# Kernel optimization log

Hardware: AMD Instinct MI355X
Metric: run time of the kernel (lower is better)

Reference implementation:

```python
import jax, jax.numpy as jnp
import numpy as np

HIDDEN = 512
HEADS = 8
HEAD_DIM = HIDDEN // HEADS
TB_HID = 32  # temporal-bias MLP hidden width


def setup_inputs() -> dict:
    key = jax.random.key(0)
    ks = jax.random.split(key, 16)
    B, S, D = 4, 1024, HIDDEN
    s = 1.0 / np.sqrt(D)
    inp = {
        "query": jax.random.normal(ks[0], (B, S, D), jnp.float32),
        "key_": jax.random.normal(ks[1], (B, S, D), jnp.float32),
        "value": jax.random.normal(ks[2], (B, S, D), jnp.float32),
        "time_delta": jax.random.uniform(ks[3], (B, S, S), jnp.float32),
        "Wq": jax.random.normal(ks[4], (D, D), jnp.float32) * s,
        "bq": jnp.zeros((D,), jnp.float32),
        "Wk": jax.random.normal(ks[5], (D, D), jnp.float32) * s,
        "bk": jnp.zeros((D,), jnp.float32),
        "Wv": jax.random.normal(ks[6], (D, D), jnp.float32) * s,
        "bv": jnp.zeros((D,), jnp.float32),
        "Wo": jax.random.normal(ks[7], (D, D), jnp.float32) * s,
        "bo": jnp.zeros((D,), jnp.float32),
        "Wt1": jax.random.normal(ks[8], (1, TB_HID), jnp.float32),
        "bt1": jnp.zeros((TB_HID,), jnp.float32),
        "Wt2": jax.random.normal(ks[9], (TB_HID, HEADS), jnp.float32) * (1.0 / np.sqrt(TB_HID)),
        "bt2": jnp.zeros((HEADS,), jnp.float32),
    }
    return inp


def reference(query, key_, value, time_delta,
              Wq, bq, Wk, bk, Wv, bv, Wo, bo, Wt1, bt1, Wt2, bt2):
    B, S, D = query.shape
    H, Hd = HEADS, HEAD_DIM
    scale = jnp.sqrt(jnp.float32(Hd))

    # projections -> [B, H, S, Hd]
    q = (query @ Wq + bq).reshape(B, S, H, Hd).transpose(0, 2, 1, 3)
    k = (key_ @ Wk + bk).reshape(B, S, H, Hd).transpose(0, 2, 1, 3)
    v = (value @ Wv + bv).reshape(B, S, H, Hd).transpose(0, 2, 1, 3)

    # content scores [B, H, S, S]
    scores = jnp.einsum('bhid,bhjd->bhij', q, k) / scale

    # temporal bias: 2-layer MLP on scalar time_delta -> per-head bias
    h = jax.nn.relu(time_delta[..., None] * Wt1[0] + bt1)   # [B, S, S, 32]
    bias = h @ Wt2 + bt2                                    # [B, S, S, H]
    scores = scores + bias.transpose(0, 3, 1, 2)

    attn = jax.nn.softmax(scores, axis=-1)  # dropout = identity (eval)
    out = jnp.einsum('bhij,bhjd->bhid', attn, v)
    out = out.transpose(0, 2, 1, 3).reshape(B, S, D)
    return out @ Wo + bo
```

## Files before the change

### kernel.cpp

```cpp
#include <hip/hip_runtime.h>

typedef _Float16 f16;
typedef _Float16 f16x4 __attribute__((ext_vector_type(4)));
typedef _Float16 f16x8 __attribute__((ext_vector_type(8)));
typedef float f32x4 __attribute__((ext_vector_type(4)));

#define L2E 1.44269504088896340736f

constexpr int D  = 512;
constexpr int S  = 1024;
constexpr int B  = 4;
constexpr int BS = B * S;

constexpr size_t OFF_WT   = 0;
constexpr size_t OFF_Q16  = OFF_WT  + 4ull * D * D * 2;
constexpr size_t OFF_K16  = OFF_Q16 + (size_t)BS * D * 2;
constexpr size_t OFF_VT   = OFF_K16 + (size_t)BS * D * 2;
constexpr size_t OFF_AT   = OFF_VT  + (size_t)BS * D * 2;
constexpr size_t OFF_TAB  = OFF_AT  + (size_t)BS * D * 2;
constexpr size_t OFF_COEF = OFF_TAB + 8ull * 1032 * 4;
constexpr size_t OFF_TDH  = OFF_COEF + 256;

__global__ __launch_bounds__(256) void prep(
    const float* __restrict__ Wq, const float* __restrict__ Wk,
    const float* __restrict__ Wv, const float* __restrict__ Wo,
    f16* __restrict__ WT,
    const float* __restrict__ td, f16* __restrict__ tdh,
    const float* __restrict__ Wt1, const float* __restrict__ bt1,
    const float* __restrict__ Wt2, const float* __restrict__ bt2,
    float* __restrict__ tab, float* __restrict__ coef)
{
    __shared__ float tile[64][65];
    __shared__ float w1s[32], b1s[32], w2s[256], b2s[8];

    const int bx = blockIdx.x;
    const int t = threadIdx.x;

    if (bx < 256) {
        const int z = bx >> 6, xy = bx & 63;
        const float* __restrict__ W = (z == 0) ? Wq : (z == 1) ? Wk : (z == 2) ? Wv : Wo;
        f16* __restrict__ out = WT + (size_t)z * D * D;
        const int k0 = (xy >> 3) * 64, n0 = (xy & 7) * 64;
        for (int i = t; i < 4096; i += 256) {
            int r = i >> 6, c = i & 63;
            tile[r][c] = W[(size_t)(k0 + r) * D + n0 + c];
        }
        __syncthreads();
        for (int i = t; i < 4096; i += 256) {
            int nn = i >> 6, kk = i & 63;
            out[(size_t)(n0 + nn) * D + k0 + kk] = (f16)tile[kk][nn];
        }
    } else if (bx < 2304) {
        const int chunk = (bx - 256) * 256 + t;
        const int row = chunk >> 7;
        const int c7 = chunk & 127;
        const int tl = c7 >> 2, gg = c7 & 3;
        const float* __restrict__ src = td + (size_t)row * S + tl * 32;
        float4 a = *reinterpret_cast<const float4*>(src + gg * 4);
        float4 c = *reinterpret_cast<const float4*>(src + 16 + gg * 4);
        f16x8 hv;
        hv[0] = (f16)a.x; hv[1] = (f16)a.y; hv[2] = (f16)a.z; hv[3] = (f16)a.w;
        hv[4] = (f16)c.x; hv[5] = (f16)c.y; hv[6] = (f16)c.z; hv[7] = (f16)c.w;
        *reinterpret_cast<f16x8*>(tdh + (size_t)chunk * 8) = hv;
    } else {
        if (t < 32) { w1s[t] = Wt1[t]; b1s[t] = bt1[t]; }
        w2s[t] = Wt2[t];
        if (t < 8) b2s[t] = bt2[t];
        __syncthreads();

        const int hh = t >> 5, j = t & 31;

        float f0 = b2s[hh], f1 = b2s[hh];
#pragma unroll 4
        for (int jj = 0; jj < 32; ++jj) {
            float w2 = w2s[jj * 8 + hh];
            f0 += fmaxf(b1s[jj], 0.f) * w2;
            f1 += fmaxf(w1s[jj] + b1s[jj], 0.f) * w2;
        }

        float devj = 0.f;
        {
            float w1 = w1s[j], b1 = b1s[j];
            float u = (w1 != 0.f) ? (-b1 / w1) : -1.f;
            if (u > 0.f && u < 1.f) {
                float fu = b2s[hh];
#pragma unroll 4
                for (int jj = 0; jj < 32; ++jj)
                    fu += fmaxf(fmaf(u, w1s[jj], b1s[jj]), 0.f) * w2s[jj * 8 + hh];
                devj = fabsf(fu - fmaf(u, f1 - f0, f0)) * L2E;
            }
        }
#pragma unroll
        for (int m = 1; m < 32; m <<= 1)
            devj = fmaxf(devj, __shfl_xor(devj, m));

        if (j == 0) {
            coef[hh]     = (f1 - f0) * L2E;
            coef[8 + hh] = f0 * L2E;
            ((int*)coef)[16 + hh] = (devj < 1e-4f) ? 1 : 0;
        }

        for (int idx = t; idx <= 1024; idx += 256) {
            float tdv = (float)idx * (1.0f / 1024.0f);
            float acc[8];
#pragma unroll
            for (int h2 = 0; h2 < 8; ++h2) acc[h2] = b2s[h2];
#pragma unroll 4
            for (int jj = 0; jj < 32; ++jj) {
                float hvv = fmaxf(fmaf(tdv, w1s[jj], b1s[jj]), 0.f);
#pragma unroll
                for (int h2 = 0; h2 < 8; ++h2) acc[h2] += hvv * w2s[jj * 8 + h2];
            }
#pragma unroll
            for (int h2 = 0; h2 < 8; ++h2)
                tab[h2 * 1032 + idx] = acc[h2] * L2E;
        }
    }
}

__global__ __launch_bounds__(256) void proj_gemm(
    const float* __restrict__ Aq, const float* __restrict__ Ak, const float* __restrict__ Av,
    const f16* __restrict__ WT,
    const float* __restrict__ bq, const float* __restrict__ bk, const float* __restrict__ bv,
    f16* __restrict__ q16, f16* __restrict__ k16, f16* __restrict__ vT, float qscale)
{
    __shared__ f16 As[2][128][40];
    __shared__ f16 Bs[2][64][40];

    const int z = blockIdx.z;
    const float* __restrict__ A    = (z == 0) ? Aq : (z == 1) ? Ak : Av;
    const float* __restrict__ bias = (z == 0) ? bq : (z == 1) ? bk : bv;
    const f16* __restrict__ W      = WT + (size_t)z * D * D;
    const float scale = (z == 0) ? qscale : 1.0f;

    const int t = threadIdx.x;
    const int l = t & 63, w = t >> 6;
    const int i16 = l & 15, g = l >> 4;
    const int wm = w >> 1, wn = w & 1;
    const int m0 = blockIdx.x * 128, n0 = blockIdx.y * 64;

    f32x4 acc[4][2] = {};

    float4 ar[4];
    f16x8  br;
    const int arow = t >> 3, ac4 = t & 7;
    const int brow = t >> 2, bc8 = t & 3;

    auto load_stage = [&](int kt) {
        const int k0 = kt * 32;
#pragma unroll
        for (int r = 0; r < 4; ++r)
            ar[r] = *reinterpret_cast<const float4*>(A + (size_t)(m0 + arow + 32 * r) * D + k0 + ac4 * 4);
        br = *reinterpret_cast<const f16x8*>(W + (size_t)(n0 + brow) * D + k0 + bc8 * 8);
    };
    auto write_stage = [&](int buf) {
#pragma unroll
        for (int r = 0; r < 4; ++r) {
            f16x4 hv;
            hv[0] = (f16)ar[r].x; hv[1] = (f16)ar[r].y; hv[2] = (f16)ar[r].z; hv[3] = (f16)ar[r].w;
            *reinterpret_cast<f16x4*>(&As[buf][arow + 32 * r][ac4 * 4]) = hv;
        }
        *reinterpret_cast<f16x8*>(&Bs[buf][brow][bc8 * 8]) = br;
    };

    load_stage(0);
    write_stage(0);
    __syncthreads();

    for (int kt = 0; kt < 16; ++kt) {
        const int cur = kt & 1;
        if (kt < 15) load_stage(kt + 1);

        f16x8 af[4], bf[2];
#pragma unroll
        for (int i = 0; i < 4; ++i)
            af[i] = *reinterpret_cast<const f16x8*>(&As[cur][wm * 64 + i * 16 + i16][g * 8]);
#pragma unroll
        for (int j = 0; j < 2; ++j)
            bf[j] = *reinterpret_cast<const f16x8*>(&Bs[cur][wn * 32 + j * 16 + i16][g * 8]);
#pragma unroll
        for (int i = 0; i < 4; ++i)
#pragma unroll
            for (int j = 0; j < 2; ++j)
                acc[i][j] = __builtin_amdgcn_mfma_f32_16x16x32_f16(af[i], bf[j], acc[i][j], 0, 0, 0);

        if (kt < 15) write_stage(cur ^ 1);
        __syncthreads();
    }

    float bvv[2];
#pragma unroll
    for (int j = 0; j < 2; ++j) bvv[j] = bias[n0 + wn * 32 + j * 16 + i16];

    if (z < 2) {
        f16* __restrict__ out = (z == 0) ? q16 : k16;
#pragma unroll
        for (int i = 0; i < 4; ++i) {
#pragma unroll
            for (int j = 0; j < 2; ++j) {
                const int nn = n0 + wn * 32 + j * 16 + i16;
#pragma unroll
                for (int e = 0; e < 4; ++e) {
                    const int mr = m0 + wm * 64 + i * 16 + g * 4 + e;
                    out[(size_t)mr * D + nn] = (f16)((acc[i][j][e] + bvv[j]) * scale);
                }
            }
        }
    } else {
#pragma unroll
        for (int i = 0; i < 4; ++i) {
            const int mr = m0 + wm * 64 + i * 16 + g * 4;
            const int bb = mr >> 10, jj = mr & 1023;
#pragma unroll
            for (int j = 0; j < 2; ++j) {
                const int nn = n0 + wn * 32 + j * 16 + i16;
                f16x4 hv;
#pragma unroll
                for (int e = 0; e < 4; ++e) hv[e] = (f16)(acc[i][j][e] + bvv[j]);
                *reinterpret_cast<f16x4*>(vT + ((size_t)(bb * D + nn)) * S + jj) = hv;
            }
        }
    }
}

__global__ __launch_bounds__(512, 4) void attn_kernel(
    const f16* __restrict__ q16, const f16* __restrict__ k16, const f16* __restrict__ vT,
    const f16* __restrict__ tdh, const float* __restrict__ tabg, const float* __restrict__ coef,
    f16* __restrict__ out16)
{
    __shared__ __align__(16) f16 Ks[2][2][2048];
    __shared__ __align__(16) f16 Vs[2][2][2048];
    __shared__ __align__(16) f16 Ps[8][512];
    __shared__ float obuf[4][16][68];
    __shared__ float mlb[4][2][16];

    const int bid = blockIdx.x;
    const int b  = bid & 3;
    const int h  = (bid >> 2) & 7;
    const int qt = bid >> 5;

    const int t = threadIdx.x;
    const int w = t >> 6, l = t & 63;
    const int i16 = l & 15, g = l >> 4;
    const int half = w >> 2, pr = w & 3;
    const int qrow = qt * 64 + pr * 16 + i16;

    const float cH = coef[h], dH = coef[8 + h];
    const int lin = ((const int*)coef)[16 + h];
    const float* __restrict__ th = tabg + h * 1032;

    f16x8 qf[2];
#pragma unroll
    for (int kf = 0; kf < 2; ++kf)
        qf[kf] = *reinterpret_cast<const f16x8*>(
            q16 + (size_t)(b * S + qrow) * D + h * 64 + kf * 32 + g * 8);

    float mr = -1e30f, lr = 0.f;
    f32x4 o[4] = {};

    const int kh   = t >> 8;
    const int krow = (t >> 3) & 31, kc8 = t & 7;
    const int vdv  = (t >> 2) & 63, vj8 = t & 3;
    const int kofs = krow * 64 + ((kc8 ^ (krow & 7)) << 3);
    const int vofs = vdv * 32 + ((vj8 ^ (vdv & 3)) << 3);
    f16x8 sk, sv;

    auto stage_load = [&](int jt) {
        sk = *reinterpret_cast<const f16x8*>(
            k16 + (size_t)(b * S + kh * 512 + jt * 32 + krow) * D + h * 64 + kc8 * 8);
        sv = *reinterpret_cast<const f16x8*>(
            vT + (size_t)(b * D + h * 64 + vdv) * S + kh * 512 + jt * 32 + vj8 * 8);
    };
    auto stage_write = [&](int buf) {
        *reinterpret_cast<f16x8*>(&Ks[buf][kh][kofs]) = sk;
        *reinterpret_cast<f16x8*>(&Vs[buf][kh][vofs]) = sv;
    };

    int kro0[2], kro1[2], vro[4];
#pragma unroll
    for (int fj = 0; fj < 2; ++fj) {
        const int rj = fj * 16 + i16;
        kro0[fj] = rj * 64 + ((g ^ (i16 & 7)) << 3);
        kro1[fj] = rj * 64 + (((g + 4) ^ (i16 & 7)) << 3);
    }
#pragma unroll
    for (int fv = 0; fv < 4; ++fv)
        vro[fv] = (fv * 16 + i16) * 32 + ((g ^ (i16 & 3)) << 3);

    const int q2  = (i16 >> 1) & 3;
    const int pw0 = i16 * 32 + ((((g >> 1)    ) ^ q2) << 3) + ((g & 1) << 2);
    const int pw1 = i16 * 32 + ((((g >> 1) + 2) ^ q2) << 3) + ((g & 1) << 2);
    const int prd = i16 * 32 + ((g ^ q2) << 3);

    const f16* __restrict__ tdp = tdh + (size_t)(b * S + qrow) * S + half * 512 + g * 8;
    f16x8 tcur, tnext;

    stage_load(0);
    tcur = *reinterpret_cast<const f16x8*>(tdp);
    stage_write(0);
    __syncthreads();

    for (int jt = 0; jt < 16; ++jt) {
        const int cur = jt & 1;
        if (jt < 15) {
            stage_load(jt + 1);
            tnext = *reinterpret_cast<const f16x8*>(tdp + (jt + 1) * 32);
        }

        f32x4 s[2];
#pragma unroll
        for (int fj = 0; fj < 2; ++fj) {
            f16x8 ka0 = *reinterpret_cast<const f16x8*>(&Ks[cur][half][kro0[fj]]);
            f16x8 ka1 = *reinterpret_cast<const f16x8*>(&Ks[cur][half][kro1[fj]]);
            f32x4 zz = {0.f, 0.f, 0.f, 0.f};
            zz = __builtin_amdgcn_mfma_f32_16x16x32_f16(ka0, qf[0], zz, 0, 0, 0);
            s[fj] = __builtin_amdgcn_mfma_f32_16x16x32_f16(ka1, qf[1], zz, 0, 0, 0);
        }

        float pvv[2][4];
        float tmax = -1e30f;
#pragma unroll
        for (int fj = 0; fj < 2; ++fj)
#pragma unroll
            for (int e = 0; e < 4; ++e) {
                float u = (float)tcur[fj * 4 + e];
                float vsc;
                if (lin) {
                    vsc = fmaf(u, cH, s[fj][e] + dH);
                } else {
                    float x = fminf(fmaxf(u, 0.f), 1.f) * 1024.f;
                    int ix = (int)x;
                    ix = (ix > 1023) ? 1023 : ix;
                    float fr = x - (float)ix;
                    float t0v = th[ix], t1v = th[ix + 1];
                    vsc = s[fj][e] + fmaf(fr, t1v - t0v, t0v);
                }
                pvv[fj][e] = vsc;
                tmax = fmaxf(tmax, vsc);
            }
        tmax = fmaxf(tmax, __shfl_xor(tmax, 16));
        tmax = fmaxf(tmax, __shfl_xor(tmax, 32));
        if (__any(tmax > mr)) {
            float mnew = fmaxf(mr, tmax);
            float alpha = exp2f(mr - mnew);
            mr = mnew;
            lr *= alpha;
#pragma unroll
            for (int fv = 0; fv < 4; ++fv) o[fv] *= alpha;
        }

        float rsum = 0.f;
        f16x4 pq[2];
#pragma unroll
        for (int fj = 0; fj < 2; ++fj)
#pragma unroll
            for (int e = 0; e < 4; ++e) {
                float p = exp2f(pvv[fj][e] - mr);
                rsum += p;
                pq[fj][e] = (f16)p;
            }
        rsum += __shfl_xor(rsum, 16);
        rsum += __shfl_xor(rsum, 32);
        lr += rsum;

        f16* ps = Ps[w];
        *reinterpret_cast<f16x4*>(ps + pw0) = pq[0];
        *reinterpret_cast<f16x4*>(ps + pw1) = pq[1];
        f16x8 pb = *reinterpret_cast<const f16x8*>(ps + prd);

#pragma unroll
        for (int fv = 0; fv < 4; ++fv) {
            f16x8 va = *reinterpret_cast<const f16x8*>(&Vs[cur][half][vro[fv]]);
            o[fv] = __builtin_amdgcn_mfma_f32_16x16x32_f16(va, pb, o[fv], 0, 0, 0);
        }

        if (jt < 15) stage_write(cur ^ 1);
        __syncthreads();
        tcur = tnext;
    }

    if (half == 1) {
#pragma unroll
        for (int fv = 0; fv < 4; ++fv)
            *reinterpret_cast<f32x4*>(&obuf[pr][i16][fv * 16 + g * 4]) = o[fv];
        if (g == 0) { mlb[pr][0][i16] = mr; mlb[pr][1][i16] = lr; }
    }
    __syncthreads();
    if (half == 0) {
        const float m1 = mlb[pr][0][i16], l1 = mlb[pr][1][i16];
        const float mm = fmaxf(mr, m1);
        const float a0 = exp2f(mr - mm), a1 = exp2f(m1 - mm);
        const float inv = 1.0f / (lr * a0 + l1 * a1);
#pragma unroll
        for (int fv = 0; fv < 4; ++fv) {
            f32x4 o1 = *reinterpret_cast<const f32x4*>(&obuf[pr][i16][fv * 16 + g * 4]);
            f16x4 hv;
#pragma unroll
            for (int e = 0; e < 4; ++e) hv[e] = (f16)((o[fv][e] * a0 + o1[e] * a1) * inv);
            *reinterpret_cast<f16x4*>(
                out16 + (size_t)(b * S + qrow) * D + h * 64 + fv * 16 + g * 4) = hv;
        }
    }
}

__global__ __launch_bounds__(256) void final_gemm(const f16* __restrict__ A, const f16* __restrict__ WoT,
                                                  const float* __restrict__ bo, float* __restrict__ out)
{
    __shared__ f16 As[2][64][40];
    __shared__ f16 Bs[2][64][40];

    const int t = threadIdx.x;
    const int l = t & 63, w = t >> 6;
    const int i16 = l & 15, g = l >> 4;
    const int wm = w >> 1, wn = w & 1;
    const int m0 = blockIdx.x * 64, n0 = blockIdx.y * 64;

    f32x4 acc[2][2] = {};
    f16x8 ar, br;
    const int srow = t >> 2, sc8 = t & 3;

    auto load_stage = [&](int kt) {
        const int k0 = kt * 32;
        ar = *reinterpret_cast<const f16x8*>(A + (size_t)(m0 + srow) * D + k0 + sc8 * 8);
        br = *reinterpret_cast<const f16x8*>(WoT + (size_t)(n0 + srow) * D + k0 + sc8 * 8);
    };
    auto write_stage = [&](int buf) {
        *reinterpret_cast<f16x8*>(&As[buf][srow][sc8 * 8]) = ar;
        *reinterpret_cast<f16x8*>(&Bs[buf][srow][sc8 * 8]) = br;
    };

    load_stage(0);
    write_stage(0);
    __syncthreads();

    for (int kt = 0; kt < 16; ++kt) {
        const int cur = kt & 1;
        if (kt < 15) load_stage(kt + 1);

        f16x8 af[2], bf[2];
#pragma unroll
        for (int i = 0; i < 2; ++i)
            af[i] = *reinterpret_cast<const f16x8*>(&As[cur][wm * 32 + i * 16 + i16][g * 8]);
#pragma unroll
        for (int j = 0; j < 2; ++j)
            bf[j] = *reinterpret_cast<const f16x8*>(&Bs[cur][wn * 32 + j * 16 + i16][g * 8]);
#pragma unroll
        for (int i = 0; i < 2; ++i)
#pragma unroll
            for (int j = 0; j < 2; ++j)
                acc[i][j] = __builtin_amdgcn_mfma_f32_16x16x32_f16(af[i], bf[j], acc[i][j], 0, 0, 0);

        if (kt < 15) write_stage(cur ^ 1);
        __syncthreads();
    }

    float bvv[2];
#pragma unroll
    for (int j = 0; j < 2; ++j) bvv[j] = bo[n0 + wn * 32 + j * 16 + i16];

#pragma unroll
    for (int i = 0; i < 2; ++i) {
#pragma unroll
        for (int j = 0; j < 2; ++j) {
            const int nn = n0 + wn * 32 + j * 16 + i16;
#pragma unroll
            for (int e = 0; e < 4; ++e) {
                const int mr = m0 + wm * 32 + i * 16 + g * 4 + e;
                out[(size_t)mr * D + nn] = acc[i][j][e] + bvv[j];
            }
        }
    }
}

extern "C" void kernel_launch(void* const* d_in, const int* in_sizes, int n_in,
                              void* d_out, int out_size, void* d_ws, size_t ws_size,
                              hipStream_t stream)
{
    (void)in_sizes; (void)n_in; (void)out_size; (void)ws_size;

    const float* query = (const float*)d_in[0];
    const float* key_  = (const float*)d_in[1];
    const float* value = (const float*)d_in[2];
    const float* td    = (const float*)d_in[3];
    const float* Wq  = (const float*)d_in[4];  const float* bq  = (const float*)d_in[5];
    const float* Wk  = (const float*)d_in[6];  const float* bk  = (const float*)d_in[7];
    const float* Wv  = (const float*)d_in[8];  const float* bv  = (const float*)d_in[9];
    const float* Wo  = (const float*)d_in[10]; const float* bo  = (const float*)d_in[11];
    const float* Wt1 = (const float*)d_in[12]; const float* bt1 = (const float*)d_in[13];
    const float* Wt2 = (const float*)d_in[14]; const float* bt2 = (const float*)d_in[15];
    float* out = (float*)d_out;

    char* ws = (char*)d_ws;
    f16*   WT   = (f16*)(ws + OFF_WT);
    f16*   q16  = (f16*)(ws + OFF_Q16);
    f16*   k16  = (f16*)(ws + OFF_K16);
    f16*   vT   = (f16*)(ws + OFF_VT);
    f16*   at16 = (f16*)(ws + OFF_AT);
    float* tab  = (float*)(ws + OFF_TAB);
    float* coef = (float*)(ws + OFF_COEF);
    f16*   tdh  = (f16*)(ws + OFF_TDH);

    prep<<<2305, 256, 0, stream>>>(Wq, Wk, Wv, Wo, WT, td, tdh,
                                   Wt1, bt1, Wt2, bt2, tab, coef);
    proj_gemm<<<dim3(32, 8, 3), 256, 0, stream>>>(query, key_, value, WT, bq, bk, bv,
                                                  q16, k16, vT, 0.125f * L2E);
    attn_kernel<<<512, 512, 0, stream>>>(q16, k16, vT, tdh, tab, coef, at16);
    final_gemm<<<dim3(64, 8), 256, 0, stream>>>(at16, WT + 3ull * (size_t)D * D, bo, out);
}
```

Measured before the change: 71.76 us.

## Replace split-KV attention with 128-row query tiles per block

```diff
diff --git a/kernel.cpp b/kernel.cpp
--- a/kernel.cpp
+++ b/kernel.cpp
@@ -223,16 +223,14 @@
     }
 }
 
-__global__ __launch_bounds__(512, 4) void attn_kernel(
+__global__ __launch_bounds__(512, 2) void attn_kernel(
     const f16* __restrict__ q16, const f16* __restrict__ k16, const f16* __restrict__ vT,
     const f16* __restrict__ tdh, const float* __restrict__ tabg, const float* __restrict__ coef,
     f16* __restrict__ out16)
 {
-    __shared__ __align__(16) f16 Ks[2][2][2048];
-    __shared__ __align__(16) f16 Vs[2][2][2048];
+    __shared__ __align__(16) f16 Ks[2][2048];
+    __shared__ __align__(16) f16 Vs[2][2048];
     __shared__ __align__(16) f16 Ps[8][512];
-    __shared__ float obuf[4][16][68];
-    __shared__ float mlb[4][2][16];
 
     const int bid = blockIdx.x;
     const int b  = bid & 3;
@@ -242,8 +240,7 @@
     const int t = threadIdx.x;
     const int w = t >> 6, l = t & 63;
     const int i16 = l & 15, g = l >> 4;
-    const int half = w >> 2, pr = w & 3;
-    const int qrow = qt * 64 + pr * 16 + i16;
+    const int qrow = qt * 128 + w * 16 + i16;
 
     const float cH = coef[h], dH = coef[8 + h];
     const int lin = ((const int*)coef)[16 + h];
@@ -258,22 +255,25 @@
     float mr = -1e30f, lr = 0.f;
     f32x4 o[4] = {};
 
-    const int kh   = t >> 8;
-    const int krow = (t >> 3) & 31, kc8 = t & 7;
-    const int vdv  = (t >> 2) & 63, vj8 = t & 3;
+    const int tk = t & 255;
+    const int isV = t >> 8;
+    const int krow = tk >> 3, kc8 = tk & 7;
+    const int vdv  = tk >> 2, vj8 = tk & 3;
     const int kofs = krow * 64 + ((kc8 ^ (krow & 7)) << 3);
     const int vofs = vdv * 32 + ((vj8 ^ (vdv & 3)) << 3);
-    f16x8 sk, sv;
+    f16x8 sg;
 
     auto stage_load = [&](int jt) {
-        sk = *reinterpret_cast<const f16x8*>(
-            k16 + (size_t)(b * S + kh * 512 + jt * 32 + krow) * D + h * 64 + kc8 * 8);
-        sv = *reinterpret_cast<const f16x8*>(
-            vT + (size_t)(b * D + h * 64 + vdv) * S + kh * 512 + jt * 32 + vj8 * 8);
+        if (!isV)
+            sg = *reinterpret_cast<const f16x8*>(
+                k16 + (size_t)(b * S + jt * 32 + krow) * D + h * 64 + kc8 * 8);
+        else
+            sg = *reinterpret_cast<const f16x8*>(
+                vT + (size_t)(b * D + h * 64 + vdv) * S + jt * 32 + vj8 * 8);
     };
     auto stage_write = [&](int buf) {
-        *reinterpret_cast<f16x8*>(&Ks[buf][kh][kofs]) = sk;
-        *reinterpret_cast<f16x8*>(&Vs[buf][kh][vofs]) = sv;
+        if (!isV) *reinterpret_cast<f16x8*>(&Ks[buf][kofs]) = sg;
+        else      *reinterpret_cast<f16x8*>(&Vs[buf][vofs]) = sg;
     };
 
     int kro0[2], kro1[2], vro[4];
@@ -292,7 +292,7 @@
     const int pw1 = i16 * 32 + ((((g >> 1) + 2) ^ q2) << 3) + ((g & 1) << 2);
     const int prd = i16 * 32 + ((g ^ q2) << 3);
 
-    const f16* __restrict__ tdp = tdh + (size_t)(b * S + qrow) * S + half * 512 + g * 8;
+    const f16* __restrict__ tdp = tdh + (size_t)(b * S + qrow) * S + g * 8;
     f16x8 tcur, tnext;
 
     stage_load(0);
@@ -300,9 +300,9 @@
     stage_write(0);
     __syncthreads();
 
-    for (int jt = 0; jt < 16; ++jt) {
+    for (int jt = 0; jt < 32; ++jt) {
         const int cur = jt & 1;
-        if (jt < 15) {
+        if (jt < 31) {
             stage_load(jt + 1);
             tnext = *reinterpret_cast<const f16x8*>(tdp + (jt + 1) * 32);
         }
@@ -310,8 +310,8 @@
         f32x4 s[2];
 #pragma unroll
         for (int fj = 0; fj < 2; ++fj) {
-            f16x8 ka0 = *reinterpret_cast<const f16x8*>(&Ks[cur][half][kro0[fj]]);
-            f16x8 ka1 = *reinterpret_cast<const f16x8*>(&Ks[cur][half][kro1[fj]]);
+            f16x8 ka0 = *reinterpret_cast<const f16x8*>(&Ks[cur][kro0[fj]]);
+            f16x8 ka1 = *reinterpret_cast<const f16x8*>(&Ks[cur][kro1[fj]]);
             f32x4 zz = {0.f, 0.f, 0.f, 0.f};
             zz = __builtin_amdgcn_mfma_f32_16x16x32_f16(ka0, qf[0], zz, 0, 0, 0);
             s[fj] = __builtin_amdgcn_mfma_f32_16x16x32_f16(ka1, qf[1], zz, 0, 0, 0);
@@ -370,36 +370,23 @@
 
 #pragma unroll
         for (int fv = 0; fv < 4; ++fv) {
-            f16x8 va = *reinterpret_cast<const f16x8*>(&Vs[cur][half][vro[fv]]);
+            f16x8 va = *reinterpret_cast<const f16x8*>(&Vs[cur][vro[fv]]);
             o[fv] = __builtin_amdgcn_mfma_f32_16x16x32_f16(va, pb, o[fv], 0, 0, 0);
         }
 
-        if (jt < 15) stage_write(cur ^ 1);
+        if (jt < 31) stage_write(cur ^ 1);
         __syncthreads();
         tcur = tnext;
     }
 
-    if (half == 1) {
-#pragma unroll
-        for (int fv = 0; fv < 4; ++fv)
-            *reinterpret_cast<f32x4*>(&obuf[pr][i16][fv * 16 + g * 4]) = o[fv];
-        if (g == 0) { mlb[pr][0][i16] = mr; mlb[pr][1][i16] = lr; }
-    }
-    __syncthreads();
-    if (half == 0) {
-        const float m1 = mlb[pr][0][i16], l1 = mlb[pr][1][i16];
-        const float mm = fmaxf(mr, m1);
-        const float a0 = exp2f(mr - mm), a1 = exp2f(m1 - mm);
-        const float inv = 1.0f / (lr * a0 + l1 * a1);
-#pragma unroll
-        for (int fv = 0; fv < 4; ++fv) {
-            f32x4 o1 = *reinterpret_cast<const f32x4*>(&obuf[pr][i16][fv * 16 + g * 4]);
-            f16x4 hv;
-#pragma unroll
-            for (int e = 0; e < 4; ++e) hv[e] = (f16)((o[fv][e] * a0 + o1[e] * a1) * inv);
-            *reinterpret_cast<f16x4*>(
-                out16 + (size_t)(b * S + qrow) * D + h * 64 + fv * 16 + g * 4) = hv;
-        }
+    const float rl = 1.f / lr;
+#pragma unroll
+    for (int fv = 0; fv < 4; ++fv) {
+        f16x4 hv;
+#pragma unroll
+        for (int e = 0; e < 4; ++e) hv[e] = (f16)(o[fv][e] * rl);
+        *reinterpret_cast<f16x4*>(
+            out16 + (size_t)(b * S + qrow) * D + h * 64 + fv * 16 + g * 4) = hv;
     }
 }
 
@@ -504,6 +491,6 @@
                                    Wt1, bt1, Wt2, bt2, tab, coef);
     proj_gemm<<<dim3(32, 8, 3), 256, 0, stream>>>(query, key_, value, WT, bq, bk, bv,
                                                   q16, k16, vT, 0.125f * L2E);
-    attn_kernel<<<512, 512, 0, stream>>>(q16, k16, vT, tdh, tab, coef, at16);
+    attn_kernel<<<256, 512, 0, stream>>>(q16, k16, vT, tdh, tab, coef, at16);
     final_gemm<<<dim3(64, 8), 256, 0, stream>>>(at16, WT + 3ull * (size_t)D * D, bo, out);
 }
```

After: 78.63 us. 1.1x slower.

## Double KV tile width per iteration in attention kernel and defer row-sum reduction

Applied to the files above, without the earlier changes.

```diff
diff --git a/kernel.cpp b/kernel.cpp
--- a/kernel.cpp
+++ b/kernel.cpp
@@ -223,15 +223,14 @@
     }
 }
 
-__global__ __launch_bounds__(512, 4) void attn_kernel(
+__global__ __launch_bounds__(512, 2) void attn_kernel(
     const f16* __restrict__ q16, const f16* __restrict__ k16, const f16* __restrict__ vT,
     const f16* __restrict__ tdh, const float* __restrict__ tabg, const float* __restrict__ coef,
     f16* __restrict__ out16)
 {
-    __shared__ __align__(16) f16 Ks[2][2][2048];
-    __shared__ __align__(16) f16 Vs[2][2][2048];
-    __shared__ __align__(16) f16 Ps[8][512];
-    __shared__ float obuf[4][16][68];
+    __shared__ __align__(16) f16 Ks[2][2][4096];
+    __shared__ __align__(16) f16 Vs[2][2][4096];
+    __shared__ __align__(16) f16 Ps[8][1024];
     __shared__ float mlb[4][2][16];
 
     const int bid = blockIdx.x;
@@ -255,134 +254,172 @@
         qf[kf] = *reinterpret_cast<const f16x8*>(
             q16 + (size_t)(b * S + qrow) * D + h * 64 + kf * 32 + g * 8);
 
-    float mr = -1e30f, lr = 0.f;
+    float mr = -1e30f, lrp = 0.f;
     f32x4 o[4] = {};
 
-    const int kh   = t >> 8;
-    const int krow = (t >> 3) & 31, kc8 = t & 7;
-    const int vdv  = (t >> 2) & 63, vj8 = t & 3;
-    const int kofs = krow * 64 + ((kc8 ^ (krow & 7)) << 3);
-    const int vofs = vdv * 32 + ((vj8 ^ (vdv & 3)) << 3);
-    f16x8 sk, sv;
-
-    auto stage_load = [&](int jt) {
-        sk = *reinterpret_cast<const f16x8*>(
-            k16 + (size_t)(b * S + kh * 512 + jt * 32 + krow) * D + h * 64 + kc8 * 8);
-        sv = *reinterpret_cast<const f16x8*>(
-            vT + (size_t)(b * D + h * 64 + vdv) * S + kh * 512 + jt * 32 + vj8 * 8);
+    int kh[2], kro_w[2], vro_w[2];
+    int krow[2], kc8[2], vdv[2], vj8[2];
+#pragma unroll
+    for (int r = 0; r < 2; ++r) {
+        int c = t + 512 * r;
+        kh[r] = c >> 9; int c9 = c & 511;
+        krow[r] = c9 >> 3; kc8[r] = c9 & 7;
+        vdv[r]  = c9 >> 3; vj8[r] = c9 & 7;
+        kro_w[r] = krow[r] * 64 + ((kc8[r] ^ (krow[r] & 7)) << 3);
+        vro_w[r] = vdv[r] * 64 + ((vj8[r] ^ (vdv[r] & 7)) << 3);
+    }
+    f16x8 sk[2], sv[2];
+
+    auto stage_load = [&](int it) {
+#pragma unroll
+        for (int r = 0; r < 2; ++r)
+            sk[r] = *reinterpret_cast<const f16x8*>(
+                k16 + (size_t)(b * S + kh[r] * 512 + it * 64 + krow[r]) * D + h * 64 + kc8[r] * 8);
+#pragma unroll
+        for (int r = 0; r < 2; ++r)
+            sv[r] = *reinterpret_cast<const f16x8*>(
+                vT + (size_t)(b * D + h * 64 + vdv[r]) * S + kh[r] * 512 + it * 64 + vj8[r] * 8);
     };
     auto stage_write = [&](int buf) {
-        *reinterpret_cast<f16x8*>(&Ks[buf][kh][kofs]) = sk;
-        *reinterpret_cast<f16x8*>(&Vs[buf][kh][vofs]) = sv;
+#pragma unroll
+        for (int r = 0; r < 2; ++r)
+            *reinterpret_cast<f16x8*>(&Ks[buf][kh[r]][kro_w[r]]) = sk[r];
+#pragma unroll
+        for (int r = 0; r < 2; ++r)
+            *reinterpret_cast<f16x8*>(&Vs[buf][kh[r]][vro_w[r]]) = sv[r];
     };
 
-    int kro0[2], kro1[2], vro[4];
-#pragma unroll
-    for (int fj = 0; fj < 2; ++fj) {
-        const int rj = fj * 16 + i16;
-        kro0[fj] = rj * 64 + ((g ^ (i16 & 7)) << 3);
-        kro1[fj] = rj * 64 + (((g + 4) ^ (i16 & 7)) << 3);
-    }
-#pragma unroll
-    for (int fv = 0; fv < 4; ++fv)
-        vro[fv] = (fv * 16 + i16) * 32 + ((g ^ (i16 & 3)) << 3);
-
-    const int q2  = (i16 >> 1) & 3;
-    const int pw0 = i16 * 32 + ((((g >> 1)    ) ^ q2) << 3) + ((g & 1) << 2);
-    const int pw1 = i16 * 32 + ((((g >> 1) + 2) ^ q2) << 3) + ((g & 1) << 2);
-    const int prd = i16 * 32 + ((g ^ q2) << 3);
+    int kro[2][2][2];
+#pragma unroll
+    for (int ss = 0; ss < 2; ++ss)
+#pragma unroll
+        for (int fj = 0; fj < 2; ++fj) {
+            const int row = ss * 32 + fj * 16 + i16;
+            kro[ss][fj][0] = row * 64 + ((g ^ (i16 & 7)) << 3);
+            kro[ss][fj][1] = row * 64 + (((g + 4) ^ (i16 & 7)) << 3);
+        }
+    int vro[2][4];
+#pragma unroll
+    for (int ss = 0; ss < 2; ++ss)
+#pragma unroll
+        for (int fv = 0; fv < 4; ++fv)
+            vro[ss][fv] = (fv * 16 + i16) * 64 + (((ss * 4 + g) ^ (i16 & 7)) << 3);
+
+    int pw[2][2], prd[2];
+#pragma unroll
+    for (int ss = 0; ss < 2; ++ss) {
+#pragma unroll
+        for (int fj = 0; fj < 2; ++fj) {
+            const int ch = ss * 4 + fj * 2 + (g >> 1);
+            pw[ss][fj] = i16 * 64 + ((ch ^ (i16 & 7)) << 3) + ((g & 1) << 2);
+        }
+        prd[ss] = i16 * 64 + (((ss * 4 + g) ^ (i16 & 7)) << 3);
+    }
 
     const f16* __restrict__ tdp = tdh + (size_t)(b * S + qrow) * S + half * 512 + g * 8;
-    f16x8 tcur, tnext;
+    f16x8 tc0, tc1, tn0, tn1;
 
     stage_load(0);
-    tcur = *reinterpret_cast<const f16x8*>(tdp);
+    tc0 = *reinterpret_cast<const f16x8*>(tdp);
+    tc1 = *reinterpret_cast<const f16x8*>(tdp + 32);
     stage_write(0);
     __syncthreads();
 
-    for (int jt = 0; jt < 16; ++jt) {
-        const int cur = jt & 1;
-        if (jt < 15) {
-            stage_load(jt + 1);
-            tnext = *reinterpret_cast<const f16x8*>(tdp + (jt + 1) * 32);
-        }
-
-        f32x4 s[2];
-#pragma unroll
-        for (int fj = 0; fj < 2; ++fj) {
-            f16x8 ka0 = *reinterpret_cast<const f16x8*>(&Ks[cur][half][kro0[fj]]);
-            f16x8 ka1 = *reinterpret_cast<const f16x8*>(&Ks[cur][half][kro1[fj]]);
-            f32x4 zz = {0.f, 0.f, 0.f, 0.f};
-            zz = __builtin_amdgcn_mfma_f32_16x16x32_f16(ka0, qf[0], zz, 0, 0, 0);
-            s[fj] = __builtin_amdgcn_mfma_f32_16x16x32_f16(ka1, qf[1], zz, 0, 0, 0);
-        }
-
-        float pvv[2][4];
+    for (int it = 0; it < 8; ++it) {
+        const int cur = it & 1;
+        if (it < 7) {
+            stage_load(it + 1);
+            tn0 = *reinterpret_cast<const f16x8*>(tdp + (it + 1) * 64);
+            tn1 = *reinterpret_cast<const f16x8*>(tdp + (it + 1) * 64 + 32);
+        }
+
+        f32x4 s[2][2];
+#pragma unroll
+        for (int ss = 0; ss < 2; ++ss)
+#pragma unroll
+            for (int fj = 0; fj < 2; ++fj) {
+                f16x8 ka0 = *reinterpret_cast<const f16x8*>(&Ks[cur][half][kro[ss][fj][0]]);
+                f16x8 ka1 = *reinterpret_cast<const f16x8*>(&Ks[cur][half][kro[ss][fj][1]]);
+                f32x4 zz = {0.f, 0.f, 0.f, 0.f};
+                zz = __builtin_amdgcn_mfma_f32_16x16x32_f16(ka0, qf[0], zz, 0, 0, 0);
+                s[ss][fj] = __builtin_amdgcn_mfma_f32_16x16x32_f16(ka1, qf[1], zz, 0, 0, 0);
+            }
+
+        float pvv[2][2][4];
         float tmax = -1e30f;
 #pragma unroll
-        for (int fj = 0; fj < 2; ++fj)
-#pragma unroll
-            for (int e = 0; e < 4; ++e) {
-                float u = (float)tcur[fj * 4 + e];
-                float vsc;
-                if (lin) {
-                    vsc = fmaf(u, cH, s[fj][e] + dH);
-                } else {
-                    float x = fminf(fmaxf(u, 0.f), 1.f) * 1024.f;
-                    int ix = (int)x;
-                    ix = (ix > 1023) ? 1023 : ix;
-                    float fr = x - (float)ix;
-                    float t0v = th[ix], t1v = th[ix + 1];
-                    vsc = s[fj][e] + fmaf(fr, t1v - t0v, t0v);
+        for (int ss = 0; ss < 2; ++ss)
+#pragma unroll
+            for (int fj = 0; fj < 2; ++fj)
+#pragma unroll
+                for (int e = 0; e < 4; ++e) {
+                    float u = (float)((ss ? tc1 : tc0)[fj * 4 + e]);
+                    float vsc;
+                    if (lin) {
+                        vsc = fmaf(u, cH, s[ss][fj][e] + dH);
+                    } else {
+                        float x = fminf(fmaxf(u, 0.f), 1.f) * 1024.f;
+                        int ix = (int)x;
+                        ix = (ix > 1023) ? 1023 : ix;
+                        float fr = x - (float)ix;
+                        float t0v = th[ix], t1v = th[ix + 1];
+                        vsc = s[ss][fj][e] + fmaf(fr, t1v - t0v, t0v);
+                    }
+                    pvv[ss][fj][e] = vsc;
+                    tmax = fmaxf(tmax, vsc);
                 }
-                pvv[fj][e] = vsc;
-                tmax = fmaxf(tmax, vsc);
-            }
         tmax = fmaxf(tmax, __shfl_xor(tmax, 16));
         tmax = fmaxf(tmax, __shfl_xor(tmax, 32));
         if (__any(tmax > mr)) {
             float mnew = fmaxf(mr, tmax);
             float alpha = exp2f(mr - mnew);
             mr = mnew;
-            lr *= alpha;
+            lrp *= alpha;
 #pragma unroll
             for (int fv = 0; fv < 4; ++fv) o[fv] *= alpha;
         }
 
-        float rsum = 0.f;
-        f16x4 pq[2];
-#pragma unroll
-        for (int fj = 0; fj < 2; ++fj)
-#pragma unroll
-            for (int e = 0; e < 4; ++e) {
-                float p = exp2f(pvv[fj][e] - mr);
-                rsum += p;
-                pq[fj][e] = (f16)p;
-            }
-        rsum += __shfl_xor(rsum, 16);
-        rsum += __shfl_xor(rsum, 32);
-        lr += rsum;
-
-        f16* ps = Ps[w];
-        *reinterpret_cast<f16x4*>(ps + pw0) = pq[0];
-        *reinterpret_cast<f16x4*>(ps + pw1) = pq[1];
-        f16x8 pb = *reinterpret_cast<const f16x8*>(ps + prd);
-
-#pragma unroll
-        for (int fv = 0; fv < 4; ++fv) {
-            f16x8 va = *reinterpret_cast<const f16x8*>(&Vs[cur][half][vro[fv]]);
-            o[fv] = __builtin_amdgcn_mfma_f32_16x16x32_f16(va, pb, o[fv], 0, 0, 0);
-        }
-
-        if (jt < 15) stage_write(cur ^ 1);
+#pragma unroll
+        for (int ss = 0; ss < 2; ++ss) {
+            f16x4 pq[2];
+#pragma unroll
+            for (int fj = 0; fj < 2; ++fj)
+#pragma unroll
+                for (int e = 0; e < 4; ++e) {
+                    float p = exp2f(pvv[ss][fj][e] - mr);
+                    lrp += p;
+                    pq[fj][e] = (f16)p;
+                }
+            f16* ps = Ps[w];
+            *reinterpret_cast<f16x4*>(ps + pw[ss][0]) = pq[0];
+            *reinterpret_cast<f16x4*>(ps + pw[ss][1]) = pq[1];
+        }
+
+#pragma unroll
+        for (int ss = 0; ss < 2; ++ss) {
+            f16x8 pb = *reinterpret_cast<const f16x8*>(&Ps[w][prd[ss]]);
+#pragma unroll
+            for (int fv = 0; fv < 4; ++fv) {
+                f16x8 va = *reinterpret_cast<const f16x8*>(&Vs[cur][half][vro[ss][fv]]);
+                o[fv] = __builtin_amdgcn_mfma_f32_16x16x32_f16(va, pb, o[fv], 0, 0, 0);
+            }
+        }
+
+        if (it < 7) stage_write(cur ^ 1);
         __syncthreads();
-        tcur = tnext;
-    }
-
+        tc0 = tn0; tc1 = tn1;
+    }
+
+    float lr = lrp;
+    lr += __shfl_xor(lr, 16);
+    lr += __shfl_xor(lr, 32);
+
+    float* ob = (float*)&Ks[0][0][0];
     if (half == 1) {
+        float* obp = ob + pr * (16 * 68);
 #pragma unroll
         for (int fv = 0; fv < 4; ++fv)
-            *reinterpret_cast<f32x4*>(&obuf[pr][i16][fv * 16 + g * 4]) = o[fv];
+            *reinterpret_cast<f32x4*>(&obp[i16 * 68 + fv * 16 + g * 4]) = o[fv];
         if (g == 0) { mlb[pr][0][i16] = mr; mlb[pr][1][i16] = lr; }
     }
     __syncthreads();
@@ -391,9 +428,10 @@
         const float mm = fmaxf(mr, m1);
         const float a0 = exp2f(mr - mm), a1 = exp2f(m1 - mm);
         const float inv = 1.0f / (lr * a0 + l1 * a1);
+        const float* obp = ob + pr * (16 * 68);
 #pragma unroll
         for (int fv = 0; fv < 4; ++fv) {
-            f32x4 o1 = *reinterpret_cast<const f32x4*>(&obuf[pr][i16][fv * 16 + g * 4]);
+            f32x4 o1 = *reinterpret_cast<const f32x4*>(&obp[i16 * 68 + fv * 16 + g * 4]);
             f16x4 hv;
 #pragma unroll
             for (int e = 0; e < 4; ++e) hv[e] = (f16)((o[fv][e] * a0 + o1[e] * a1) * inv);
```

Measured after the change: 76.72 us. +6.9%, slower.
